# Kernel tuning notes

Hardware: AMD Instinct MI355X
Metric: run time of the kernel (lower is better)

The kernel has to match this reference:

```python
import jax, jax.numpy as jnp
import numpy as np

D_MODEL = 512
NHEAD = 8
HEAD_DIM = D_MODEL // NHEAD
DFF = 2048
KSIZE = 3
EPS = 1e-5


def conv1d(x, w, b, pad):
    # x: [B, Cin, S], w: [Cout, Cin, K] -> [B, Cout, S]
    y = jax.lax.conv_general_dilated(x, w, window_strides=(1,), padding=[(pad, pad)],
                                     dimension_numbers=("NCH", "OIH", "NCH"))
    return y + b[None, :, None]


def layernorm(x, g, b):
    mu = jnp.mean(x, axis=-1, keepdims=True)
    var = jnp.mean(jnp.square(x - mu), axis=-1, keepdims=True)
    return (x - mu) * jax.lax.rsqrt(var + EPS) * g + b


def setup_inputs() -> dict:
    key = jax.random.key(0)
    ks = jax.random.split(key, 16)
    B, S = 8, 1024
    # conv init: normal(0, sqrt(2/(K*out_ch))) per head (out_ch = HEAD_DIM), bias 0.1
    sq = np.sqrt(2.0 / (KSIZE * HEAD_DIM)).astype(np.float32)
    sv = np.sqrt(2.0 / (1 * HEAD_DIM)).astype(np.float32)
    inp = {
        "src": jax.random.normal(ks[0], (B, S, D_MODEL), jnp.float32),
        "Wq": jax.random.normal(ks[1], (D_MODEL, D_MODEL, KSIZE), jnp.float32) * sq,
        "bq": jnp.full((D_MODEL,), 0.1, jnp.float32),
        "Wk": jax.random.normal(ks[2], (D_MODEL, D_MODEL, KSIZE), jnp.float32) * sq,
        "bk": jnp.full((D_MODEL,), 0.1, jnp.float32),
        "Wv": jax.random.normal(ks[3], (D_MODEL, D_MODEL, 1), jnp.float32) * sv,
        "bv": jnp.full((D_MODEL,), 0.1, jnp.float32),
        "Wo": jax.random.normal(ks[4], (D_MODEL, D_MODEL), jnp.float32) * 0.02,
        "bo": jnp.zeros((D_MODEL,), jnp.float32),
        "W1": jax.random.normal(ks[5], (DFF, D_MODEL), jnp.float32) * 0.02,
        "b1": jnp.zeros((DFF,), jnp.float32),
        "W2": jax.random.normal(ks[6], (D_MODEL, DFF), jnp.float32) * 0.02,
        "b2": jnp.zeros((D_MODEL,), jnp.float32),
        "g1": jnp.ones((D_MODEL,), jnp.float32),
        "be1": jnp.zeros((D_MODEL,), jnp.float32),
        "g2": jnp.ones((D_MODEL,), jnp.float32),
        "be2": jnp.zeros((D_MODEL,), jnp.float32),
    }
    return inp


def reference(src, Wq, bq, Wk, bk, Wv, bv, Wo, bo, W1, b1, W2, b2, g1, be1, g2, be2):
    B, S, D = src.shape
    H, hd = NHEAD, HEAD_DIM
    xt = jnp.transpose(src, (0, 2, 1))  # [B, D, S]
    # H per-head convs over the same input == one conv with D output channels
    q = conv1d(xt, Wq, bq, (KSIZE - 1) // 2).reshape(B, H, hd, S)
    k = conv1d(xt, Wk, bk, (KSIZE - 1) // 2).reshape(B, H, hd, S)
    v = conv1d(xt, Wv, bv, 0).reshape(B, H, hd, S)
    # NOTE: source divides by head_dim (not sqrt(head_dim))
    scores = jnp.einsum("bhds,bhdt->bhst", q, k) / hd
    att = jax.nn.softmax(scores, axis=-1)  # [B, H, S, S]
    av = jnp.einsum("bhst,bhdt->bhsd", att, v)  # [B, H, S, hd]
    av = jnp.transpose(av, (0, 2, 1, 3)).reshape(B, S, D)
    sa = av @ Wo.T + bo
    x = layernorm(src + sa, g1, be1)  # post-norm (norm_first=False)
    ff = jax.nn.relu(x @ W1.T + b1) @ W2.T + b2
    return layernorm(x + ff, g2, be2)
```

## Files before the change

### kernel.cpp

```cpp
#include <hip/hip_runtime.h>
#include <hip/hip_bf16.h>

using bf16 = __hip_bfloat16;
typedef __attribute__((ext_vector_type(8))) short s8v;
typedef __attribute__((ext_vector_type(4))) short s4v;
typedef __attribute__((ext_vector_type(4))) float f32x4;

#define DEV __device__ __forceinline__

DEV f32x4 mfma16(s8v a, s8v b, f32x4 c) {
    return __builtin_amdgcn_mfma_f32_16x16x32_bf16(a, b, c, 0, 0, 0);
}

DEV void gl_to_lds16(const bf16* g, bf16* l) {
    __builtin_amdgcn_global_load_lds(
        (const __attribute__((address_space(1))) void*)g,
        (__attribute__((address_space(3))) void*)l, 16, 0, 0);
}

DEV unsigned short bfbits(bf16 h) { union { bf16 h; unsigned short u; } c; c.h = h; return c.u; }
DEV unsigned pk2(float a, float b) {
    return (unsigned)bfbits(__float2bfloat16(a)) | ((unsigned)bfbits(__float2bfloat16(b)) << 16);
}
DEV unsigned pk2t(float a, float b) {
    return (__float_as_uint(a) >> 16) | (__float_as_uint(b) & 0xffff0000u);
}
DEV void unpk8(uint4 u, float* x) {
    const unsigned uu[4] = {u.x, u.y, u.z, u.w};
#pragma unroll
    for (int j = 0; j < 4; j++) {
        x[2 * j]     = __uint_as_float(uu[j] << 16);
        x[2 * j + 1] = __uint_as_float(uu[j] & 0xffff0000u);
    }
}

__global__ __launch_bounds__(256)
void prep_all(const float* __restrict__ src, const float* __restrict__ Wv,
              const float* __restrict__ Wo, const float* __restrict__ W1,
              const float* __restrict__ W2, const float* __restrict__ Wq,
              const float* __restrict__ Wk, bf16* __restrict__ srcb,
              bf16* __restrict__ Wvb, bf16* __restrict__ Wob, bf16* __restrict__ W1b,
              bf16* __restrict__ W2b, bf16* __restrict__ WqT, bf16* __restrict__ WkT,
              bf16* __restrict__ zp) {
    const int bid = blockIdx.x;
    if (bid < 6656) {
        const long long i4 = ((long long)bid * 256 + threadIdx.x) * 4;
        const float* in;
        bf16* outp;
        long long off;
        if (i4 < 4194304)      { in = src; outp = srcb; off = 0; }
        else if (i4 < 4456448) { in = Wv;  outp = Wvb;  off = 4194304; }
        else if (i4 < 4718592) { in = Wo;  outp = Wob;  off = 4456448; }
        else if (i4 < 5767168) { in = W1;  outp = W1b;  off = 4718592; }
        else                   { in = W2;  outp = W2b;  off = 5767168; }
        const long long j = i4 - off;
        const float4 v = *(const float4*)(in + j);
        uint2 o;
        o.x = pk2(v.x, v.y);
        o.y = pk2(v.z, v.w);
        *(uint2*)(outp + j) = o;
    } else {
        const int i = (bid - 6656) * 256 + threadIdx.x;
        if (i < 512) zp[i] = __float2bfloat16(0.f);
        const int dk = i >> 18, rem = i & 262143, co = rem >> 9, ci = rem & 511;
        const size_t s = (size_t)co * 1536 + ci * 3 + dk;
        WqT[i] = __float2bfloat16(Wq[s]);
        WkT[i] = __float2bfloat16(Wk[s]);
    }
}

__global__ __launch_bounds__(256)
void conv_qk(const bf16* __restrict__ src, const bf16* __restrict__ WqT,
             const bf16* __restrict__ WkT, const float* __restrict__ bq,
             const float* __restrict__ bk, bf16* __restrict__ Qo, bf16* __restrict__ Ko,
             const bf16* __restrict__ zp) {
    const int z = blockIdx.z, b = z & 7, isK = z >> 3;
    const bf16* WT = isK ? WkT : WqT;
    const float* bias = isK ? bk : bq;
    bf16* out = isK ? Ko : Qo;
    const float qs = isK ? 1.0f : 0.022542109951390054f;
    const bf16* S = src + ((size_t)b << 19);
    const int m0 = blockIdx.x * 128, n0 = blockIdx.y * 128;
    const int tid = threadIdx.x, w = tid >> 6, l = tid & 63;
    const int lq = l & 15, quad = l >> 4;
    const int wm = (w >> 1) << 6, wn = (w & 1) << 6;
    __shared__ __align__(16) bf16 As[4224], Bs[12288];
    f32x4 acc[4][4] = {};
    for (int ci0 = 0; ci0 < 512; ci0 += 32) {
        if (ci0) __syncthreads();
#pragma unroll
        for (int j = 0; j < 2; j++) {
            const int r = j * 64 + w * 16 + (l >> 2);
            const int srow = m0 - 1 + r;
            const bf16* ga = (srow >= 0 && srow < 1024)
                                 ? S + (size_t)srow * 512 + ci0 + (l & 3) * 8
                                 : zp + (l & 3) * 8;
            gl_to_lds16(ga, &As[(j * 64 + w * 16) * 32]);
        }
        if (tid < 8) {
            const int srow = m0 + 127 + (l >> 2);
            const bf16* ga = (srow < 1024) ? S + (size_t)srow * 512 + ci0 + (l & 3) * 8
                                           : zp + (l & 3) * 8;
            gl_to_lds16(ga, &As[128 * 32]);
        }
#pragma unroll
        for (int dk = 0; dk < 3; dk++)
#pragma unroll
            for (int j = 0; j < 2; j++) {
                const int co = n0 + j * 64 + w * 16 + (l >> 2);
                gl_to_lds16(WT + ((size_t)dk << 18) + (size_t)co * 512 + ci0 + (l & 3) * 8,
                            &Bs[dk * 4096 + (j * 64 + w * 16) * 32]);
            }
        __syncthreads();
#pragma unroll
        for (int dk = 0; dk < 3; dk++) {
            s8v af[4], bfv[4];
#pragma unroll
            for (int x = 0; x < 4; x++) {
                af[x]  = *(const s8v*)&As[(wm + x * 16 + lq + dk) * 32 + quad * 8];
                bfv[x] = *(const s8v*)&Bs[dk * 4096 + (wn + x * 16 + lq) * 32 + quad * 8];
            }
#pragma unroll
            for (int mt = 0; mt < 4; mt++)
#pragma unroll
                for (int nt = 0; nt < 4; nt++)
                    acc[mt][nt] = mfma16(af[mt], bfv[nt], acc[mt][nt]);
        }
    }
#pragma unroll
    for (int nt = 0; nt < 4; nt++) {
        const int co = n0 + wn + nt * 16 + lq;
        const float bn = bias[co];
        const size_t obase = ((size_t)b << 19) + ((size_t)(co >> 6) << 16) + (co & 63);
#pragma unroll
        for (int mt = 0; mt < 4; mt++)
#pragma unroll
            for (int r = 0; r < 4; r++) {
                const int s = m0 + wm + mt * 16 + quad * 4 + r;
                out[obase + (size_t)s * 64] = __float2bfloat16((acc[mt][nt][r] + bn) * qs);
            }
    }
}

template <int EPI>
__global__ __launch_bounds__(256)
void gemm_nt(const bf16* __restrict__ A, const bf16* __restrict__ B,
             const float* __restrict__ bias, void* __restrict__ C, int M, int N, int K,
             int lda, int ldb, int ldc, long long aOff, long long bOff, long long cOff) {
    const int m0 = blockIdx.x * 128, n0 = blockIdx.y * 128, z = blockIdx.z;
    A += (size_t)z * aOff;
    B += (size_t)z * bOff;
    const int tid = threadIdx.x, w = tid >> 6, l = tid & 63;
    const int lq = l & 15, quad = l >> 4;
    const int wm = (w >> 1) << 6, wn = (w & 1) << 6;
    __shared__ __align__(16) bf16 As[8192], Bs[8192];
    f32x4 acc[4][4] = {};
    const int srow = w * 8 + (l >> 3), scol = (l & 7) * 8;
    for (int k0 = 0; k0 < K; k0 += 64) {
        if (k0) __syncthreads();
#pragma unroll
        for (int j = 0; j < 4; j++) {
            gl_to_lds16(A + (size_t)(m0 + j * 32 + srow) * lda + k0 + scol,
                        &As[(j * 32 + w * 8) * 64]);
            gl_to_lds16(B + (size_t)(n0 + j * 32 + srow) * ldb + k0 + scol,
                        &Bs[(j * 32 + w * 8) * 64]);
        }
        __syncthreads();
#pragma unroll
        for (int ks = 0; ks < 2; ks++) {
            s8v af[4], bfv[4];
#pragma unroll
            for (int x = 0; x < 4; x++) {
                af[x]  = *(const s8v*)&As[(wm + x * 16 + lq) * 64 + ks * 32 + quad * 8];
                bfv[x] = *(const s8v*)&Bs[(wn + x * 16 + lq) * 64 + ks * 32 + quad * 8];
            }
#pragma unroll
            for (int mt = 0; mt < 4; mt++)
#pragma unroll
                for (int nt = 0; nt < 4; nt++)
                    acc[mt][nt] = mfma16(af[mt], bfv[nt], acc[mt][nt]);
        }
    }
#pragma unroll
    for (int nt = 0; nt < 4; nt++) {
        const int n = n0 + wn + nt * 16 + lq;
        const float bn = (EPI == 1) ? bias[n] : 0.f;
#pragma unroll
        for (int mt = 0; mt < 4; mt++)
#pragma unroll
            for (int r = 0; r < 4; r++) {
                const int m = m0 + wm + mt * 16 + quad * 4 + r;
                float v = acc[mt][nt][r];
                const size_t off = (size_t)z * cOff + (size_t)m * ldc + n;
                if (EPI == 3) {
                    ((float*)C)[off] = v;
                } else {
                    v += (EPI == 2) ? bias[m] : bn;
                    if (EPI == 1) v = fmaxf(v, 0.f);
                    ((bf16*)C)[off] = __float2bfloat16(v);
                }
            }
    }
}

__global__ __launch_bounds__(256)
void attn_kernel(const bf16* __restrict__ Q, const bf16* __restrict__ K,
                 const bf16* __restrict__ V, bf16* __restrict__ av) {
    const int bh = blockIdx.x, b = bh >> 3, h = bh & 7;
    const bf16* Qp = Q + ((size_t)bh << 16);
    const bf16* Kp = K + ((size_t)bh << 16);
    const bf16* Vp = V + ((size_t)bh << 16);
    const int tid = threadIdx.x, w = tid >> 6, l = tid & 63;
    const int lq = l & 15, quad = l >> 4;
    const int q0 = blockIdx.y * 128 + w * 16;
    __shared__ __align__(16) bf16 Ks[4096], Vs[4096], Ps[8192];
    bf16* Pw0 = &Ps[(w * 2 + 0) * 1024];
    bf16* Pw1 = &Ps[(w * 2 + 1) * 1024];
    const s8v qf00 = *(const s8v*)&Qp[(size_t)(q0 + lq) * 64 + quad * 8];
    const s8v qf01 = *(const s8v*)&Qp[(size_t)(q0 + lq) * 64 + 32 + quad * 8];
    const s8v qf10 = *(const s8v*)&Qp[(size_t)(q0 + 64 + lq) * 64 + quad * 8];
    const s8v qf11 = *(const s8v*)&Qp[(size_t)(q0 + 64 + lq) * 64 + 32 + quad * 8];
    f32x4 o0[4] = {}, o1[4] = {};
    float l0 = 0.f, l1 = 0.f;
    const int sr = tid >> 3;
    const int scb = tid & 7;
    const int swz_st = (scb ^ (sr & 7)) * 8;
    const int rdz0 = (quad ^ (lq & 7)) * 8;
    const int rdz1 = ((quad + 4) ^ (lq & 7)) * 8;
    const int pwz = ((quad >> 1) ^ (lq & 7)) * 8 + (quad & 1) * 4;
    s8v kA = *(const s8v*)&Kp[(size_t)sr * 64 + scb * 8];
    s8v kB = *(const s8v*)&Kp[(size_t)(sr + 32) * 64 + scb * 8];
    s8v vA = *(const s8v*)&Vp[(size_t)sr * 1024 + scb * 8];
    s8v vB = *(const s8v*)&Vp[(size_t)(sr + 32) * 1024 + scb * 8];
    for (int t0 = 0; t0 < 1024; t0 += 64) {
        __syncthreads();
        *(s8v*)&Ks[sr * 64 + swz_st] = kA;
        *(s8v*)&Ks[(sr + 32) * 64 + swz_st] = kB;
        *(s8v*)&Vs[sr * 64 + swz_st] = vA;
        *(s8v*)&Vs[(sr + 32) * 64 + swz_st] = vB;
        if (t0 + 64 < 1024) {
            const int t1 = t0 + 64;
            kA = *(const s8v*)&Kp[(size_t)(t1 + sr) * 64 + scb * 8];
            kB = *(const s8v*)&Kp[(size_t)(t1 + sr + 32) * 64 + scb * 8];
            vA = *(const s8v*)&Vp[(size_t)sr * 1024 + t1 + scb * 8];
            vB = *(const s8v*)&Vp[(size_t)(sr + 32) * 1024 + t1 + scb * 8];
        }
        __syncthreads();
        f32x4 st0[4] = {}, st1[4] = {};
#pragma unroll
        for (int tt = 0; tt < 4; tt++) {
            const int rb = (tt * 16 + lq) * 64;
            const s8v ka0 = *(const s8v*)&Ks[rb + rdz0];
            const s8v ka1 = *(const s8v*)&Ks[rb + rdz1];
            st0[tt] = mfma16(ka0, qf00, st0[tt]);
            st0[tt] = mfma16(ka1, qf01, st0[tt]);
            st1[tt] = mfma16(ka0, qf10, st1[tt]);
            st1[tt] = mfma16(ka1, qf11, st1[tt]);
        }
        float cs0 = 0.f, cs1 = 0.f;
#pragma unroll
        for (int tt = 0; tt < 4; tt++) {
            const float a0 = __builtin_amdgcn_exp2f(st0[tt][0]);
            const float a1 = __builtin_amdgcn_exp2f(st0[tt][1]);
            const float a2 = __builtin_amdgcn_exp2f(st0[tt][2]);
            const float a3 = __builtin_amdgcn_exp2f(st0[tt][3]);
            cs0 += (a0 + a1) + (a2 + a3);
            uint2 pkv;
            pkv.x = pk2t(a0, a1);
            pkv.y = pk2t(a2, a3);
            *(uint2*)&Pw0[lq * 64 + (pwz ^ (tt * 16))] = pkv;
            const float b0 = __builtin_amdgcn_exp2f(st1[tt][0]);
            const float b1 = __builtin_amdgcn_exp2f(st1[tt][1]);
            const float b2 = __builtin_amdgcn_exp2f(st1[tt][2]);
            const float b3 = __builtin_amdgcn_exp2f(st1[tt][3]);
            cs1 += (b0 + b1) + (b2 + b3);
            uint2 pkw;
            pkw.x = pk2t(b0, b1);
            pkw.y = pk2t(b2, b3);
            *(uint2*)&Pw1[lq * 64 + (pwz ^ (tt * 16))] = pkw;
        }
        cs0 += __shfl_xor(cs0, 16);
        cs0 += __shfl_xor(cs0, 32);
        cs1 += __shfl_xor(cs1, 16);
        cs1 += __shfl_xor(cs1, 32);
        l0 += cs0;
        l1 += cs1;
        const s8v pb00 = *(const s8v*)&Pw0[lq * 64 + rdz0];
        const s8v pb01 = *(const s8v*)&Pw0[lq * 64 + rdz1];
        const s8v pb10 = *(const s8v*)&Pw1[lq * 64 + rdz0];
        const s8v pb11 = *(const s8v*)&Pw1[lq * 64 + rdz1];
#pragma unroll
        for (int dt = 0; dt < 4; dt++) {
            const int rb = (dt * 16 + lq) * 64;
            const s8v va0 = *(const s8v*)&Vs[rb + rdz0];
            const s8v va1 = *(const s8v*)&Vs[rb + rdz1];
            o0[dt] = mfma16(va0, pb00, o0[dt]);
            o0[dt] = mfma16(va1, pb01, o0[dt]);
            o1[dt] = mfma16(va0, pb10, o1[dt]);
            o1[dt] = mfma16(va1, pb11, o1[dt]);
        }
    }
    const float i0 = 1.f / l0, i1 = 1.f / l1;
    const size_t rb0 = ((size_t)b * 1024 + q0 + lq) * 512 + h * 64;
    const size_t rb1 = rb0 + (size_t)64 * 512;
#pragma unroll
    for (int dt = 0; dt < 4; dt++) {
        uint2 ov;
        ov.x = pk2(o0[dt][0] * i0, o0[dt][1] * i0);
        ov.y = pk2(o0[dt][2] * i0, o0[dt][3] * i0);
        *(uint2*)&av[rb0 + dt * 16 + quad * 4] = ov;
        uint2 ow;
        ow.x = pk2(o1[dt][0] * i1, o1[dt][1] * i1);
        ow.y = pk2(o1[dt][2] * i1, o1[dt][3] * i1);
        *(uint2*)&av[rb1 + dt * 16 + quad * 4] = ow;
    }
}

template <int MODE>
__global__ __launch_bounds__(256)
void ln_kernel(const void* __restrict__ A, const float* __restrict__ P0,
               const float* __restrict__ P1, const float* __restrict__ bias,
               const float* __restrict__ g, const float* __restrict__ be,
               void* __restrict__ outp) {
    const int w = threadIdx.x >> 6, l = threadIdx.x & 63;
    const size_t row = (size_t)blockIdx.x * 4 + w;
    const size_t base = row * 512 + l * 8;
    float x[8];
    if (MODE == 1) {
        const float4 a0 = *(const float4*)((const float*)A + base);
        const float4 a1 = *(const float4*)((const float*)A + base + 4);
        x[0] = a0.x; x[1] = a0.y; x[2] = a0.z; x[3] = a0.w;
        x[4] = a1.x; x[5] = a1.y; x[6] = a1.z; x[7] = a1.w;
    } else {
        unpk8(*(const uint4*)((const bf16*)A + base), x);
    }
    const float4 p00 = *(const float4*)(P0 + base);
    const float4 p01 = *(const float4*)(P0 + base + 4);
    const float4 p10 = *(const float4*)(P1 + base);
    const float4 p11 = *(const float4*)(P1 + base + 4);
    const float4 bb0 = *(const float4*)(bias + l * 8);
    const float4 bb1 = *(const float4*)(bias + l * 8 + 4);
    x[0] += p00.x + p10.x + bb0.x; x[1] += p00.y + p10.y + bb0.y;
    x[2] += p00.z + p10.z + bb0.z; x[3] += p00.w + p10.w + bb0.w;
    x[4] += p01.x + p11.x + bb1.x; x[5] += p01.y + p11.y + bb1.y;
    x[6] += p01.z + p11.z + bb1.z; x[7] += p01.w + p11.w + bb1.w;
    float s = 0.f, sq = 0.f;
#pragma unroll
    for (int j = 0; j < 8; j++) { s += x[j]; sq += x[j] * x[j]; }
#pragma unroll
    for (int off = 1; off < 64; off <<= 1) {
        s += __shfl_xor(s, off);
        sq += __shfl_xor(sq, off);
    }
    const float mean = s * (1.f / 512.f);
    const float var = sq * (1.f / 512.f) - mean * mean;
    const float rstd = rsqrtf(fmaxf(var, 0.f) + 1e-5f);
    const float4 g0 = *(const float4*)(g + l * 8);
    const float4 g1 = *(const float4*)(g + l * 8 + 4);
    const float4 e0 = *(const float4*)(be + l * 8);
    const float4 e1 = *(const float4*)(be + l * 8 + 4);
    const float gv[8] = {g0.x, g0.y, g0.z, g0.w, g1.x, g1.y, g1.z, g1.w};
    const float ev[8] = {e0.x, e0.y, e0.z, e0.w, e1.x, e1.y, e1.z, e1.w};
    float y[8];
#pragma unroll
    for (int j = 0; j < 8; j++) y[j] = (x[j] - mean) * rstd * gv[j] + ev[j];
    if (MODE == 1) {
        uint4 o;
        o.x = pk2(y[0], y[1]); o.y = pk2(y[2], y[3]);
        o.z = pk2(y[4], y[5]); o.w = pk2(y[6], y[7]);
        *(uint4*)((bf16*)outp + base) = o;
    } else {
        *(float4*)((float*)outp + base)     = make_float4(y[0], y[1], y[2], y[3]);
        *(float4*)((float*)outp + base + 4) = make_float4(y[4], y[5], y[6], y[7]);
    }
}

extern "C" void kernel_launch(void* const* d_in, const int* in_sizes, int n_in, void* d_out,
                              int out_size, void* d_ws, size_t ws_size, hipStream_t stream) {
    const float* src = (const float*)d_in[0];
    const float* Wq = (const float*)d_in[1];
    const float* bq = (const float*)d_in[2];
    const float* Wk = (const float*)d_in[3];
    const float* bk = (const float*)d_in[4];
    const float* Wv = (const float*)d_in[5];
    const float* bv = (const float*)d_in[6];
    const float* Wo = (const float*)d_in[7];
    const float* bo = (const float*)d_in[8];
    const float* W1 = (const float*)d_in[9];
    const float* b1 = (const float*)d_in[10];
    const float* W2 = (const float*)d_in[11];
    const float* b2 = (const float*)d_in[12];
    const float* g1 = (const float*)d_in[13];
    const float* be1 = (const float*)d_in[14];
    const float* g2 = (const float*)d_in[15];
    const float* be2 = (const float*)d_in[16];
    float* out = (float*)d_out;

    char* base = (char*)d_ws;
    bf16* srcb = (bf16*)(base + 0);
    bf16* Qb   = (bf16*)(base + 8388608);
    bf16* Kb   = (bf16*)(base + 16777216);
    bf16* Vb   = (bf16*)(base + 25165824);
    bf16* ff1  = (bf16*)(base + 0);
    bf16* avb  = (bf16*)(base + 33554432);
    bf16* xb   = avb;
    float* saf = (float*)(base + 41943040);
    bf16* WqT  = (bf16*)(base + 75497472);
    bf16* WkT  = (bf16*)(base + 77070336);
    bf16* zp   = (bf16*)(base + 78643200);
    bf16* Wvb  = (bf16*)(base + 78644224);
    bf16* Wob  = (bf16*)(base + 79168512);
    bf16* W1b  = (bf16*)(base + 79692800);
    bf16* W2b  = (bf16*)(base + 81789952);

    prep_all<<<9728, 256, 0, stream>>>(src, Wv, Wo, W1, W2, Wq, Wk, srcb, Wvb, Wob, W1b,
                                       W2b, WqT, WkT, zp);
    conv_qk<<<dim3(8, 4, 16), 256, 0, stream>>>(srcb, WqT, WkT, bq, bk, Qb, Kb, zp);
    gemm_nt<2><<<dim3(4, 8, 8), 256, 0, stream>>>(Wvb, srcb, bv, Vb, 512, 1024, 512,
                                                  512, 512, 1024, 0, 524288, 524288);
    attn_kernel<<<dim3(64, 8), 256, 0, stream>>>(Qb, Kb, Vb, avb);
    gemm_nt<3><<<dim3(64, 4, 2), 256, 0, stream>>>(avb, Wob, nullptr, saf, 8192, 512, 256,
                                                   512, 512, 512, 256, 256, 4194304LL);
    ln_kernel<1><<<2048, 256, 0, stream>>>(src, saf, saf + 4194304, bo, g1, be1, xb);
    gemm_nt<1><<<dim3(64, 16, 1), 256, 0, stream>>>(xb, W1b, b1, ff1, 8192, 2048, 512,
                                                    512, 512, 2048, 0, 0, 0);
    gemm_nt<3><<<dim3(64, 4, 2), 256, 0, stream>>>(ff1, W2b, nullptr, saf, 8192, 512, 1024,
                                                   2048, 2048, 512, 1024, 1024, 4194304LL);
    ln_kernel<2><<<2048, 256, 0, stream>>>(xb, saf, saf + 4194304, b2, g2, be2, out);
}
```

Measured before the change: 266.4 us.

## Merge V projection into conv launch and halve attention query tile per block

```diff
diff --git a/kernel.cpp b/kernel.cpp
--- a/kernel.cpp
+++ b/kernel.cpp
@@ -70,75 +70,127 @@
 }
 
 __global__ __launch_bounds__(256)
-void conv_qk(const bf16* __restrict__ src, const bf16* __restrict__ WqT,
-             const bf16* __restrict__ WkT, const float* __restrict__ bq,
-             const float* __restrict__ bk, bf16* __restrict__ Qo, bf16* __restrict__ Ko,
-             const bf16* __restrict__ zp) {
-    const int z = blockIdx.z, b = z & 7, isK = z >> 3;
-    const bf16* WT = isK ? WkT : WqT;
-    const float* bias = isK ? bk : bq;
-    bf16* out = isK ? Ko : Qo;
-    const float qs = isK ? 1.0f : 0.022542109951390054f;
-    const bf16* S = src + ((size_t)b << 19);
-    const int m0 = blockIdx.x * 128, n0 = blockIdx.y * 128;
+void conv_v(const bf16* __restrict__ src, const bf16* __restrict__ WqT,
+            const bf16* __restrict__ WkT, const float* __restrict__ bq,
+            const float* __restrict__ bk, bf16* __restrict__ Qo, bf16* __restrict__ Ko,
+            const bf16* __restrict__ zp, const bf16* __restrict__ Wvb,
+            const float* __restrict__ bv, bf16* __restrict__ Vb) {
+    const int z = blockIdx.z;
     const int tid = threadIdx.x, w = tid >> 6, l = tid & 63;
     const int lq = l & 15, quad = l >> 4;
     const int wm = (w >> 1) << 6, wn = (w & 1) << 6;
-    __shared__ __align__(16) bf16 As[4224], Bs[12288];
-    f32x4 acc[4][4] = {};
-    for (int ci0 = 0; ci0 < 512; ci0 += 32) {
-        if (ci0) __syncthreads();
-#pragma unroll
-        for (int j = 0; j < 2; j++) {
-            const int r = j * 64 + w * 16 + (l >> 2);
-            const int srow = m0 - 1 + r;
-            const bf16* ga = (srow >= 0 && srow < 1024)
-                                 ? S + (size_t)srow * 512 + ci0 + (l & 3) * 8
-                                 : zp + (l & 3) * 8;
-            gl_to_lds16(ga, &As[(j * 64 + w * 16) * 32]);
-        }
-        if (tid < 8) {
-            const int srow = m0 + 127 + (l >> 2);
-            const bf16* ga = (srow < 1024) ? S + (size_t)srow * 512 + ci0 + (l & 3) * 8
-                                           : zp + (l & 3) * 8;
-            gl_to_lds16(ga, &As[128 * 32]);
-        }
-#pragma unroll
-        for (int dk = 0; dk < 3; dk++)
+    __shared__ __align__(16) bf16 smem[16896];
+    if (z < 16) {
+        const int b = z & 7, isK = z >> 3;
+        const bf16* WT = isK ? WkT : WqT;
+        const float* bias = isK ? bk : bq;
+        bf16* out = isK ? Ko : Qo;
+        const float qs = isK ? 1.0f : 0.022542109951390054f;
+        const bf16* S = src + ((size_t)b << 19);
+        const int m0 = blockIdx.x * 128, n0 = blockIdx.y * 128;
+        bf16* As = smem;
+        bf16* Bs = smem + 4224;
+        f32x4 acc[4][4] = {};
+        for (int ci0 = 0; ci0 < 512; ci0 += 32) {
+            if (ci0) __syncthreads();
 #pragma unroll
             for (int j = 0; j < 2; j++) {
-                const int co = n0 + j * 64 + w * 16 + (l >> 2);
-                gl_to_lds16(WT + ((size_t)dk << 18) + (size_t)co * 512 + ci0 + (l & 3) * 8,
-                            &Bs[dk * 4096 + (j * 64 + w * 16) * 32]);
-            }
-        __syncthreads();
-#pragma unroll
-        for (int dk = 0; dk < 3; dk++) {
-            s8v af[4], bfv[4];
-#pragma unroll
-            for (int x = 0; x < 4; x++) {
-                af[x]  = *(const s8v*)&As[(wm + x * 16 + lq + dk) * 32 + quad * 8];
-                bfv[x] = *(const s8v*)&Bs[dk * 4096 + (wn + x * 16 + lq) * 32 + quad * 8];
-            }
+                const int r = j * 64 + w * 16 + (l >> 2);
+                const int srow = m0 - 1 + r;
+                const bf16* ga = (srow >= 0 && srow < 1024)
+                                     ? S + (size_t)srow * 512 + ci0 + (l & 3) * 8
+                                     : zp + (l & 3) * 8;
+                gl_to_lds16(ga, &As[(j * 64 + w * 16) * 32]);
+            }
+            if (tid < 8) {
+                const int srow = m0 + 127 + (l >> 2);
+                const bf16* ga = (srow < 1024) ? S + (size_t)srow * 512 + ci0 + (l & 3) * 8
+                                               : zp + (l & 3) * 8;
+                gl_to_lds16(ga, &As[128 * 32]);
+            }
+#pragma unroll
+            for (int dk = 0; dk < 3; dk++)
+#pragma unroll
+                for (int j = 0; j < 2; j++) {
+                    const int co = n0 + j * 64 + w * 16 + (l >> 2);
+                    gl_to_lds16(WT + ((size_t)dk << 18) + (size_t)co * 512 + ci0 + (l & 3) * 8,
+                                &Bs[dk * 4096 + (j * 64 + w * 16) * 32]);
+                }
+            __syncthreads();
+#pragma unroll
+            for (int dk = 0; dk < 3; dk++) {
+                s8v af[4], bfv[4];
+#pragma unroll
+                for (int x = 0; x < 4; x++) {
+                    af[x]  = *(const s8v*)&As[(wm + x * 16 + lq + dk) * 32 + quad * 8];
+                    bfv[x] = *(const s8v*)&Bs[dk * 4096 + (wn + x * 16 + lq) * 32 + quad * 8];
+                }
+#pragma unroll
+                for (int mt = 0; mt < 4; mt++)
+#pragma unroll
+                    for (int nt = 0; nt < 4; nt++)
+                        acc[mt][nt] = mfma16(af[mt], bfv[nt], acc[mt][nt]);
+            }
+        }
+#pragma unroll
+        for (int nt = 0; nt < 4; nt++) {
+            const int co = n0 + wn + nt * 16 + lq;
+            const float bn = bias[co];
+            const size_t obase = ((size_t)b << 19) + ((size_t)(co >> 6) << 16) + (co & 63);
 #pragma unroll
             for (int mt = 0; mt < 4; mt++)
 #pragma unroll
-                for (int nt = 0; nt < 4; nt++)
-                    acc[mt][nt] = mfma16(af[mt], bfv[nt], acc[mt][nt]);
-        }
-    }
-#pragma unroll
-    for (int nt = 0; nt < 4; nt++) {
-        const int co = n0 + wn + nt * 16 + lq;
-        const float bn = bias[co];
-        const size_t obase = ((size_t)b << 19) + ((size_t)(co >> 6) << 16) + (co & 63);
-#pragma unroll
-        for (int mt = 0; mt < 4; mt++)
-#pragma unroll
-            for (int r = 0; r < 4; r++) {
-                const int s = m0 + wm + mt * 16 + quad * 4 + r;
-                out[obase + (size_t)s * 64] = __float2bfloat16((acc[mt][nt][r] + bn) * qs);
-            }
+                for (int r = 0; r < 4; r++) {
+                    const int s = m0 + wm + mt * 16 + quad * 4 + r;
+                    out[obase + (size_t)s * 64] = __float2bfloat16((acc[mt][nt][r] + bn) * qs);
+                }
+        }
+    } else {
+        const int b = z - 16;
+        const bf16* A = Wvb;
+        const bf16* B = src + (size_t)b * 524288;
+        bf16* C = Vb + (size_t)b * 524288;
+        const int m0 = blockIdx.y * 128, n0 = blockIdx.x * 128;
+        bf16* As = smem;
+        bf16* Bs = smem + 8192;
+        f32x4 acc[4][4] = {};
+        const int srow = w * 8 + (l >> 3), scol = (l & 7) * 8;
+        for (int k0 = 0; k0 < 512; k0 += 64) {
+            if (k0) __syncthreads();
+#pragma unroll
+            for (int j = 0; j < 4; j++) {
+                gl_to_lds16(A + (size_t)(m0 + j * 32 + srow) * 512 + k0 + scol,
+                            &As[(j * 32 + w * 8) * 64]);
+                gl_to_lds16(B + (size_t)(n0 + j * 32 + srow) * 512 + k0 + scol,
+                            &Bs[(j * 32 + w * 8) * 64]);
+            }
+            __syncthreads();
+#pragma unroll
+            for (int ks = 0; ks < 2; ks++) {
+                s8v af[4], bfv[4];
+#pragma unroll
+                for (int x = 0; x < 4; x++) {
+                    af[x]  = *(const s8v*)&As[(wm + x * 16 + lq) * 64 + ks * 32 + quad * 8];
+                    bfv[x] = *(const s8v*)&Bs[(wn + x * 16 + lq) * 64 + ks * 32 + quad * 8];
+                }
+#pragma unroll
+                for (int mt = 0; mt < 4; mt++)
+#pragma unroll
+                    for (int nt = 0; nt < 4; nt++)
+                        acc[mt][nt] = mfma16(af[mt], bfv[nt], acc[mt][nt]);
+            }
+        }
+#pragma unroll
+        for (int nt = 0; nt < 4; nt++) {
+            const int n = n0 + wn + nt * 16 + lq;
+#pragma unroll
+            for (int mt = 0; mt < 4; mt++)
+#pragma unroll
+                for (int r = 0; r < 4; r++) {
+                    const int m = m0 + wm + mt * 16 + quad * 4 + r;
+                    C[(size_t)m * 1024 + n] = __float2bfloat16(acc[mt][nt][r] + bv[m]);
+                }
+        }
     }
 }
 
@@ -195,7 +247,7 @@
                 if (EPI == 3) {
                     ((float*)C)[off] = v;
                 } else {
-                    v += (EPI == 2) ? bias[m] : bn;
+                    v += bn;
                     if (EPI == 1) v = fmaxf(v, 0.f);
                     ((bf16*)C)[off] = __float2bfloat16(v);
                 }
@@ -212,16 +264,13 @@
     const bf16* Vp = V + ((size_t)bh << 16);
     const int tid = threadIdx.x, w = tid >> 6, l = tid & 63;
     const int lq = l & 15, quad = l >> 4;
-    const int q0 = blockIdx.y * 128 + w * 16;
-    __shared__ __align__(16) bf16 Ks[4096], Vs[4096], Ps[8192];
-    bf16* Pw0 = &Ps[(w * 2 + 0) * 1024];
-    bf16* Pw1 = &Ps[(w * 2 + 1) * 1024];
-    const s8v qf00 = *(const s8v*)&Qp[(size_t)(q0 + lq) * 64 + quad * 8];
-    const s8v qf01 = *(const s8v*)&Qp[(size_t)(q0 + lq) * 64 + 32 + quad * 8];
-    const s8v qf10 = *(const s8v*)&Qp[(size_t)(q0 + 64 + lq) * 64 + quad * 8];
-    const s8v qf11 = *(const s8v*)&Qp[(size_t)(q0 + 64 + lq) * 64 + 32 + quad * 8];
-    f32x4 o0[4] = {}, o1[4] = {};
-    float l0 = 0.f, l1 = 0.f;
+    const int q0 = blockIdx.y * 64 + w * 16;
+    __shared__ __align__(16) bf16 Ks[4096], Vs[4096], Ps[4096];
+    bf16* Pw = &Ps[w * 1024];
+    const s8v qf0 = *(const s8v*)&Qp[(size_t)(q0 + lq) * 64 + quad * 8];
+    const s8v qf1 = *(const s8v*)&Qp[(size_t)(q0 + lq) * 64 + 32 + quad * 8];
+    f32x4 o[4] = {};
+    float l0 = 0.f;
     const int sr = tid >> 3;
     const int scb = tid & 7;
     const int swz_st = (scb ^ (sr & 7)) * 8;
@@ -246,73 +295,50 @@
             vB = *(const s8v*)&Vp[(size_t)(sr + 32) * 1024 + t1 + scb * 8];
         }
         __syncthreads();
-        f32x4 st0[4] = {}, st1[4] = {};
+        f32x4 st[4] = {};
 #pragma unroll
         for (int tt = 0; tt < 4; tt++) {
             const int rb = (tt * 16 + lq) * 64;
             const s8v ka0 = *(const s8v*)&Ks[rb + rdz0];
             const s8v ka1 = *(const s8v*)&Ks[rb + rdz1];
-            st0[tt] = mfma16(ka0, qf00, st0[tt]);
-            st0[tt] = mfma16(ka1, qf01, st0[tt]);
-            st1[tt] = mfma16(ka0, qf10, st1[tt]);
-            st1[tt] = mfma16(ka1, qf11, st1[tt]);
-        }
-        float cs0 = 0.f, cs1 = 0.f;
+            st[tt] = mfma16(ka0, qf0, st[tt]);
+            st[tt] = mfma16(ka1, qf1, st[tt]);
+        }
+        float cs0 = 0.f;
 #pragma unroll
         for (int tt = 0; tt < 4; tt++) {
-            const float a0 = __builtin_amdgcn_exp2f(st0[tt][0]);
-            const float a1 = __builtin_amdgcn_exp2f(st0[tt][1]);
-            const float a2 = __builtin_amdgcn_exp2f(st0[tt][2]);
-            const float a3 = __builtin_amdgcn_exp2f(st0[tt][3]);
+            const float a0 = __builtin_amdgcn_exp2f(st[tt][0]);
+            const float a1 = __builtin_amdgcn_exp2f(st[tt][1]);
+            const float a2 = __builtin_amdgcn_exp2f(st[tt][2]);
+            const float a3 = __builtin_amdgcn_exp2f(st[tt][3]);
             cs0 += (a0 + a1) + (a2 + a3);
             uint2 pkv;
             pkv.x = pk2t(a0, a1);
             pkv.y = pk2t(a2, a3);
-            *(uint2*)&Pw0[lq * 64 + (pwz ^ (tt * 16))] = pkv;
-            const float b0 = __builtin_amdgcn_exp2f(st1[tt][0]);
-            const float b1 = __builtin_amdgcn_exp2f(st1[tt][1]);
-            const float b2 = __builtin_amdgcn_exp2f(st1[tt][2]);
-            const float b3 = __builtin_amdgcn_exp2f(st1[tt][3]);
-            cs1 += (b0 + b1) + (b2 + b3);
-            uint2 pkw;
-            pkw.x = pk2t(b0, b1);
-            pkw.y = pk2t(b2, b3);
-            *(uint2*)&Pw1[lq * 64 + (pwz ^ (tt * 16))] = pkw;
+            *(uint2*)&Pw[lq * 64 + (pwz ^ (tt * 16))] = pkv;
         }
         cs0 += __shfl_xor(cs0, 16);
         cs0 += __shfl_xor(cs0, 32);
-        cs1 += __shfl_xor(cs1, 16);
-        cs1 += __shfl_xor(cs1, 32);
         l0 += cs0;
-        l1 += cs1;
-        const s8v pb00 = *(const s8v*)&Pw0[lq * 64 + rdz0];
-        const s8v pb01 = *(const s8v*)&Pw0[lq * 64 + rdz1];
-        const s8v pb10 = *(const s8v*)&Pw1[lq * 64 + rdz0];
-        const s8v pb11 = *(const s8v*)&Pw1[lq * 64 + rdz1];
+        const s8v pb0 = *(const s8v*)&Pw[lq * 64 + rdz0];
+        const s8v pb1 = *(const s8v*)&Pw[lq * 64 + rdz1];
 #pragma unroll
         for (int dt = 0; dt < 4; dt++) {
             const int rb = (dt * 16 + lq) * 64;
             const s8v va0 = *(const s8v*)&Vs[rb + rdz0];
             const s8v va1 = *(const s8v*)&Vs[rb + rdz1];
-            o0[dt] = mfma16(va0, pb00, o0[dt]);
-            o0[dt] = mfma16(va1, pb01, o0[dt]);
-            o1[dt] = mfma16(va0, pb10, o1[dt]);
-            o1[dt] = mfma16(va1, pb11, o1[dt]);
-        }
-    }
-    const float i0 = 1.f / l0, i1 = 1.f / l1;
+            o[dt] = mfma16(va0, pb0, o[dt]);
+            o[dt] = mfma16(va1, pb1, o[dt]);
+        }
+    }
+    const float i0 = 1.f / l0;
     const size_t rb0 = ((size_t)b * 1024 + q0 + lq) * 512 + h * 64;
-    const size_t rb1 = rb0 + (size_t)64 * 512;
 #pragma unroll
     for (int dt = 0; dt < 4; dt++) {
         uint2 ov;
-        ov.x = pk2(o0[dt][0] * i0, o0[dt][1] * i0);
-        ov.y = pk2(o0[dt][2] * i0, o0[dt][3] * i0);
+        ov.x = pk2(o[dt][0] * i0, o[dt][1] * i0);
+        ov.y = pk2(o[dt][2] * i0, o[dt][3] * i0);
         *(uint2*)&av[rb0 + dt * 16 + quad * 4] = ov;
-        uint2 ow;
-        ow.x = pk2(o1[dt][0] * i1, o1[dt][1] * i1);
-        ow.y = pk2(o1[dt][2] * i1, o1[dt][3] * i1);
-        *(uint2*)&av[rb1 + dt * 16 + quad * 4] = ow;
     }
 }
 
@@ -415,10 +441,9 @@
 
     prep_all<<<9728, 256, 0, stream>>>(src, Wv, Wo, W1, W2, Wq, Wk, srcb, Wvb, Wob, W1b,
                                        W2b, WqT, WkT, zp);
-    conv_qk<<<dim3(8, 4, 16), 256, 0, stream>>>(srcb, WqT, WkT, bq, bk, Qb, Kb, zp);
-    gemm_nt<2><<<dim3(4, 8, 8), 256, 0, stream>>>(Wvb, srcb, bv, Vb, 512, 1024, 512,
-                                                  512, 512, 1024, 0, 524288, 524288);
-    attn_kernel<<<dim3(64, 8), 256, 0, stream>>>(Qb, Kb, Vb, avb);
+    conv_v<<<dim3(8, 4, 24), 256, 0, stream>>>(srcb, WqT, WkT, bq, bk, Qb, Kb, zp,
+                                               Wvb, bv, Vb);
+    attn_kernel<<<dim3(64, 16), 256, 0, stream>>>(Qb, Kb, Vb, avb);
     gemm_nt<3><<<dim3(64, 4, 2), 256, 0, stream>>>(avb, Wob, nullptr, saf, 8192, 512, 256,
                                                    512, 512, 512, 256, 256, 4194304LL);
     ln_kernel<1><<<2048, 256, 0, stream>>>(src, saf, saf + 4194304, bo, g1, be1, xb);
```

After: 261.0 us. 1.02x faster.
